# Kernel tuning notes

Hardware: AMD Instinct MI355X
Metric: run time of the kernel (lower is better)

The kernel has to match this reference:

```python
import jax, jax.numpy as jnp
import numpy as np
jax.config.update("jax_enable_x64", True)  # subchunk uses float64 decays (T=128 > 24)

B, T, D = 4, 2048, 1024
H, K = 16, 64            # head_size = 64, D = H*K
CHUNK = 128              # T % 128 == 0 -> only the 128-chunk path of _chunked_wkv runs
DMIX, DDEC = 32, 64      # D_MIX_DIM, D_DECAY_DIM
PREC_MIN = 0.005
LN_EPS = 1e-5 * 8.0 ** 2 # eps * head_size_divisor**2


def setup_inputs() -> dict:
    key = jax.random.key(0)
    ks = jax.random.split(key, 24)
    f32 = jnp.float32
    rn = lambda k, s, sc=1.0: (jax.random.normal(k, s) * sc).astype(f32)
    un = lambda k, s, lo, hi: jax.random.uniform(k, s, minval=lo, maxval=hi).astype(f32)
    inv_sq = 1.0 / np.sqrt(D)
    return {
        "x": rn(ks[0], (B, T, D)),
        # token-mix interpolation coefficients (init-like: in [0,1])
        "time_maa_x": un(ks[1], (1, 1, D), 0.0, 1.0),
        "time_maa_w": un(ks[2], (1, 1, D), 0.0, 1.0),
        "time_maa_k": un(ks[3], (1, 1, D), 0.0, 1.0),
        "time_maa_v": un(ks[4], (1, 1, D), 0.0, 1.0),
        "time_maa_r": un(ks[5], (1, 1, D), 0.0, 1.0),
        "time_maa_g": un(ks[6], (1, 1, D), 0.0, 1.0),
        "time_maa_w1": rn(ks[7], (D, 5 * DMIX), 0.01),
        "time_maa_w2": un(ks[8], (5, DMIX, D), -0.01, 0.01),
        # decay: init range roughly [-6, -1] like the module
        "time_decay": un(ks[9], (1, 1, D), -6.0, -1.0),
        "time_decay_w1": rn(ks[10], (D, DDEC), 0.01),
        "time_decay_w2": un(ks[11], (DDEC, D), -0.01, 0.01),
        "time_faaaa": un(ks[12], (H, K), -0.1, 0.5),
        # projections (stored [in, out]; x @ W == nn.Linear)
        "Wr": rn(ks[13], (D, D), inv_sq),
        "Wk": rn(ks[14], (D, D), inv_sq),
        "Wv": rn(ks[15], (D, D), inv_sq),
        "Wg": rn(ks[16], (D, D), inv_sq),
        "Wo": rn(ks[17], (D, D), inv_sq),
        "ln_w": jnp.ones((D,), f32),
        "ln_b": jnp.zeros((D,), f32),
    }


def _causal_shift(x):
    # x[t-1], zero at t=0
    return jnp.pad(x[:, :-1, :], ((0, 0), (1, 0), (0, 0)))


def _chunked_wkv(r, k, v, w, u, state):
    # r,k,v,w: [B,H,L,K]; u: [1,H,1,K]; state: [B,H,K,V]
    Bb, Hh, L, Kk = r.shape
    V = v.shape[-1]
    Tc = CHUNK
    N = L // Tc
    f64 = jnp.float64

    w_decay = jnp.clip(jnp.exp(w), PREC_MIN, None)
    wc_log = jnp.log(w_decay.astype(jnp.float32)).reshape(Bb, Hh, N, Tc, Kk)
    wc_cum = jnp.cumsum(wc_log, axis=-2)                              # inclusive cumsum over chunk
    shifted = jnp.pad(wc_cum[..., :-1, :], ((0, 0),) * 3 + ((1, 0), (0, 0)))
    ws = wc_log.sum(axis=-2, keepdims=True)                           # [B,H,N,1,K] total log-decay
    w_inter = jnp.exp(ws - wc_cum).astype(r.dtype)
    w_intra = jnp.exp(wc_cum - wc_log).astype(r.dtype)

    rc = r.reshape(Bb, Hh, N, Tc, Kk)
    kc = k.reshape(Bb, Hh, N, Tc, Kk)
    vc = v.reshape(Bb, Hh, N, Tc, V)

    # intra-chunk attention in float64 with mid-chunk offset for stability
    off = shifted[..., Tc // 2:Tc // 2 + 1, :]
    r_decay = jnp.exp((shifted - off).astype(f64))
    k_inv = jnp.exp((off - wc_cum).astype(f64))
    a = jnp.einsum('bhnik,bhnjk->bhnij', rc.astype(f64) * r_decay,
                   kc.astype(f64) * k_inv).astype(r.dtype)
    a = jnp.tril(a, -1)
    diag = jnp.einsum('bhntk,bhntk->bhnt', rc, u[:, :, :, None, :] * kc)  # u bonus on the diagonal
    a = a + diag[..., None] * jnp.eye(Tc, dtype=r.dtype)
    out = jnp.einsum('bhnij,bhnjv->bhniv', a, vc)

    # inter-chunk recurrent state carry
    wkv = jnp.einsum('bhntk,bhntv->bhnkv', kc * w_inter, vc)          # per-chunk KV update
    ws_e = jnp.swapaxes(jnp.exp(ws), -1, -2).astype(r.dtype)          # [B,H,N,K,1]

    def step(s, xs):
        wkv_i, ws_i = xs
        return s * ws_i + wkv_i, s                                    # emit state BEFORE update

    state_f, states = jax.lax.scan(step, state,
                                   (jnp.moveaxis(wkv, 2, 0), jnp.moveaxis(ws_e, 2, 0)))
    states = jnp.moveaxis(states, 0, 2)                               # [B,H,N,K,V]
    out = out + jnp.einsum('bhntk,bhnkv->bhntv', rc * w_intra, states)
    return out.reshape(Bb, Hh, L, V), state_f


def reference(x, time_maa_x, time_maa_w, time_maa_k, time_maa_v, time_maa_r,
              time_maa_g, time_maa_w1, time_maa_w2, time_decay, time_decay_w1,
              time_decay_w2, time_faaaa, Wr, Wk, Wv, Wg, Wo, ln_w, ln_b):
    Bb, Tt, Dd = x.shape
    xx = _causal_shift(x) - x                                          # dxprev (recurrent mode)

    # data-dependent 5-way token-mix (RWKV-6 LoRA mix)
    xxx = jnp.tanh((x + xx * time_maa_x) @ time_maa_w1)                # [B,T,5*DMIX]
    m = jnp.einsum('btfi,fid->fbtd', xxx.reshape(Bb, Tt, 5, DMIX), time_maa_w2)
    mw, mk, mv, mr, mg = m
    xw = x + xx * (time_maa_w + mw)
    xk = x + xx * (time_maa_k + mk)
    xv = x + xx * (time_maa_v + mv)
    xr = x + xx * (time_maa_r + mr)
    xg = x + xx * (time_maa_g + mg)

    to_heads = lambda t: t.reshape(Bb, Tt, H, K).transpose(0, 2, 1, 3)  # [B,H,T,K]
    r = to_heads(xr @ Wr)
    k = to_heads(xk @ Wk)
    v = to_heads(xv @ Wv)
    g = jax.nn.silu(xg @ Wg)

    ww = time_decay + jnp.tanh(xw @ time_decay_w1) @ time_decay_w2
    w = to_heads(-jnp.exp(ww))                                         # log-decay (negative)
    u = time_faaaa.reshape(1, H, 1, K)

    state0 = jnp.zeros((Bb, H, K, K), dtype=x.dtype)
    out, _state = _chunked_wkv(r, k, v, w, u, state0)

    # GroupNorm(n_head groups) over flattened (B*T, D)
    og = out.transpose(0, 2, 1, 3).reshape(Bb * Tt, H, K)
    mu = og.mean(-1, keepdims=True)
    var = og.var(-1, keepdims=True)
    og = (og - mu) / jnp.sqrt(var + LN_EPS)
    out = (og.reshape(Bb * Tt, Dd) * ln_w + ln_b).reshape(Bb, Tt, Dd)

    return (out * g) @ Wo
```

## Files before the change

kernel.cpp:

```cpp
#include <hip/hip_runtime.h>
#include <hip/hip_bf16.h>
#include <math.h>
#include <stdint.h>

typedef __hip_bfloat16 bf16;
typedef __attribute__((ext_vector_type(8))) short short8;
typedef __attribute__((ext_vector_type(4))) short short4v;
typedef __attribute__((ext_vector_type(4))) float f32x4;

#define Tt 2048
#define Dd 1024
#define Hh 16

__device__ __forceinline__ float b2f(bf16 v){ return __bfloat162float(v); }
__device__ __forceinline__ bf16  f2b(float v){ return __float2bfloat16(v); }

__device__ __forceinline__ void async16(const void* g, void* l){
  __builtin_amdgcn_global_load_lds(
      (__attribute__((address_space(1))) void*)(g),
      (__attribute__((address_space(3))) void*)(l),
      16, 0, 0);
}

__device__ __forceinline__ int seg_t(int lr, int t0, int Lm1){ return t0 + (lr & Lm1); }
__device__ __forceinline__ size_t seg_grow(int lr, int b0, int t0, int Llog2, int Lm1){
  return ((size_t)(b0 + (lr >> Llog2)) * Tt) + (size_t)seg_t(lr, t0, Lm1);
}

__device__ __forceinline__ void xcd_swz(int& bn, int& bm, int& z){
  int nbm = gridDim.y;
  if((nbm & 7) == 0){
    int flat = blockIdx.x + (blockIdx.y << 3) + blockIdx.z * (nbm << 3);
    int j = flat & 7, k = flat >> 3;
    int cs = nbm >> 3;
    bn = (k & 7) << 7;
    int kk = k >> 3;
    bm = (j * cs + (kk % cs)) << 7;
    z  = kk / cs;
  } else {
    bn = blockIdx.x << 7; bm = blockIdx.y << 7; z = blockIdx.z;
  }
}

struct MixP { const bf16* maa[5]; bf16* dst[5]; };
struct Proj4 { const bf16* A[4]; const bf16* Bt[4]; bf16* C[4]; };
struct ConvP { const void* src[20]; bf16* dst[20]; };
struct T5P  { const bf16* src[5]; bf16* dst[5]; };

__global__ __launch_bounds__(256) void k_detect(const unsigned short* __restrict__ xs,
                                                int* __restrict__ flag){
  __shared__ int bad;
  if(threadIdx.x == 0) bad = 0;
  __syncthreads();
  int local = 0;
  for(int i = threadIdx.x; i < 8192; i += 256){
    unsigned e = (xs[i] >> 7) & 0xFF;
    if(e >= 0xC0) local++;
  }
  if(local) atomicAdd(&bad, local);
  __syncthreads();
  if(threadIdx.x == 0) flag[0] = (bad > 16) ? 1 : 0;
}

__global__ __launch_bounds__(256) void k_conv_all(ConvP p, const int* __restrict__ flag){
  const int PRE[21] = {0,8388608,8389632,8390656,8391680,8392704,8393728,8394752,
                       8558592,8722432,8723456,8788992,8854528,8855552,9904128,
                       10952704,12001280,13049856,14098432,14099456,14100480};
  int v = (blockIdx.x * 256 + threadIdx.x) * 4;
  if(v >= 14100480) return;
  int a = 0;
  #pragma unroll
  for(int i = 1; i < 20; i++) if(v >= PRE[i]) a = i;
  int off = v - PRE[a];
  bf16* d = p.dst[a] + off;
  if(flag[0]){
    f32x4 xv = *(const f32x4*)((const float*)p.src[a] + off);
    short4v o;
    #pragma unroll
    for(int j = 0; j < 4; j++) ((bf16*)&o)[j] = f2b(xv[j]);
    *(short4v*)d = o;
  } else {
    *(short4v*)d = *(const short4v*)((const short*)p.src[a] + off);
  }
}

__global__ __launch_bounds__(256) void k_transpose5(T5P p){
  __shared__ bf16 tile[32][33];
  const bf16* __restrict__ src = p.src[blockIdx.z];
  bf16* __restrict__ dst       = p.dst[blockIdx.z];
  int bx = blockIdx.x * 32, by = blockIdx.y * 32;
  int tx = threadIdx.x & 31, ty = threadIdx.x >> 5;
  for(int r = ty; r < 32; r += 8)
    tile[r][tx] = src[(size_t)(by + r) * 1024 + bx + tx];
  __syncthreads();
  for(int r = ty; r < 32; r += 8)
    dst[(size_t)(bx + r) * 1024 + by + tx] = tile[tx][r];
}

__global__ __launch_bounds__(256) void k_transposeP(const bf16* __restrict__ src,
                                                    bf16* __restrict__ dst,
                                                    int K, int N, int Npad){
  int idx = blockIdx.x * 256 + threadIdx.x;
  if(idx >= Npad * K) return;
  int n = idx / K, k = idx - n * K;
  dst[idx] = (n < N) ? src[(size_t)k * N + n] : f2b(0.f);
}

__global__ __launch_bounds__(256) void k_transposeP5(const bf16* __restrict__ src,
                                                     bf16* __restrict__ dst){
  int z = blockIdx.z;
  int idx = blockIdx.x * 256 + threadIdx.x;
  int n = idx >> 5, k = idx & 31;
  dst[(size_t)z * 32768 + idx] = src[(size_t)z * 32768 + (size_t)k * 1024 + n];
}

__global__ __launch_bounds__(256) void k_prep(const bf16* __restrict__ x,
                                              const bf16* __restrict__ tmx,
                                              bf16* __restrict__ xmx,
                                              int b0, int t0, int Llog2){
  const int Lm1 = (1 << Llog2) - 1;
  int idx = blockIdx.x * 256 + threadIdx.x;
  int lr = idx >> 10, d = idx & 1023;
  size_t grow = seg_grow(lr, b0, t0, Llog2, Lm1);
  int tl = seg_t(lr, t0, Lm1);
  float xc = b2f(x[grow * Dd + d]);
  float xp = tl ? b2f(x[(grow - 1) * Dd + d]) : 0.f;
  xmx[idx] = f2b(xc + (xp - xc) * b2f(tmx[d]));
}

constexpr int GEPI_BF16 = 0, GEPI_SILU = 1, GEPI_OUT = 2;

template<int EPI>
__global__ __launch_bounds__(256) void gemm_mfma(
    const bf16* __restrict__ A,
    const bf16* __restrict__ Bt,
    void* __restrict__ Cv,
    const int* __restrict__ oflag,
    int rowoff){
  __shared__ __align__(16) short As[128 * 32];
  __shared__ __align__(16) short Bs[128 * 32];
  int tid = threadIdx.x;
  int bn, bm, zz;
  xcd_swz(bn, bm, zz);
  int w = tid >> 6, lane = tid & 63;
  int wm = (w & 1) * 64, wn = (w >> 1) * 64;
  int m16 = lane & 15, quad = lane >> 4;

  f32x4 acc[4][4];
  #pragma unroll
  for(int mi = 0; mi < 4; mi++)
    #pragma unroll
    for(int ni = 0; ni < 4; ni++)
      acc[mi][ni] = (f32x4){0.f, 0.f, 0.f, 0.f};

  int srow = tid >> 2;
  int sk8  = (tid & 3) * 8;
  const bf16* Ag = A  + (size_t)(bm + srow) * 1024 + sk8;
  const bf16* Bg = Bt + (size_t)(bn + srow) * 1024 + sk8;
  short* Al = As + w * 512;
  short* Bl = Bs + w * 512;

  for(int kb = 0; kb < 1024; kb += 32){
    #pragma unroll
    for(int rep = 0; rep < 2; rep++){
      async16(Ag + (size_t)rep * 64 * 1024 + kb, Al + rep * 2048);
      async16(Bg + (size_t)rep * 64 * 1024 + kb, Bl + rep * 2048);
    }
    __syncthreads();
    short8 af[4], bfr[4];
    #pragma unroll
    for(int mi = 0; mi < 4; mi++)
      af[mi] = *(const short8*)(As + (wm + mi * 16 + m16) * 32 + quad * 8);
    #pragma unroll
    for(int ni = 0; ni < 4; ni++)
      bfr[ni] = *(const short8*)(Bs + (wn + ni * 16 + m16) * 32 + quad * 8);
    #pragma unroll
    for(int mi = 0; mi < 4; mi++)
      #pragma unroll
      for(int ni = 0; ni < 4; ni++)
        acc[mi][ni] = __builtin_amdgcn_mfma_f32_16x16x32_bf16(af[mi], bfr[ni], acc[mi][ni], 0, 0, 0);
    __syncthreads();
  }
  #pragma unroll
  for(int mi = 0; mi < 4; mi++){
    #pragma unroll
    for(int ni = 0; ni < 4; ni++){
      #pragma unroll
      for(int r = 0; r < 4; r++){
        int row = bm + wm + mi * 16 + quad * 4 + r;
        int col = bn + wn + ni * 16 + m16;
        float v = acc[mi][ni][r];
        if constexpr(EPI == GEPI_BF16){
          ((bf16*)Cv)[(size_t)row * 1024 + col] = f2b(v);
        } else if constexpr(EPI == GEPI_SILU){
          ((bf16*)Cv)[(size_t)row * 1024 + col] = f2b(v / (1.f + expf(-v)));
        } else {
          size_t off = (size_t)(row + rowoff) * 1024 + col;
          if(oflag[0]) ((float*)Cv)[off] = v;
          else         ((bf16*)Cv)[off]  = f2b(v);
        }
      }
    }
  }
}

__global__ __launch_bounds__(512) void gemm_proj4(Proj4 prm){
  __shared__ __align__(16) short As[2][256 * 32];
  __shared__ __align__(16) short Bs[2][256 * 32];
  int tid = threadIdx.x;
  int flat = blockIdx.x + (blockIdx.y << 2) + (blockIdx.z << 7);
  int j = flat & 7, k = flat >> 3;
  int bn = (k & 3) << 8;
  int kk = k >> 2;
  int bm = (j * 4 + (kk & 3)) << 8;
  int z  = kk >> 2;
  const bf16* __restrict__ A  = prm.A[z];
  const bf16* __restrict__ Bt = prm.Bt[z];
  bf16* __restrict__ C        = prm.C[z];
  int w = tid >> 6, lane = tid & 63;
  int wm = (w & 1) * 128, wn = (w >> 1) * 64;
  int m16 = lane & 15, quad = lane >> 4;

  f32x4 acc[8][4];
  #pragma unroll
  for(int mi = 0; mi < 8; mi++)
    #pragma unroll
    for(int ni = 0; ni < 4; ni++)
      acc[mi][ni] = (f32x4){0.f, 0.f, 0.f, 0.f};

  int srow = tid >> 2;
  int c4   = ((tid & 3) - (srow >> 1)) & 3;
  const bf16* Ag = A  + (size_t)(bm + srow) * 1024 + c4 * 8;
  const bf16* Bg = Bt + (size_t)(bn + srow) * 1024 + c4 * 8;

  auto STG = [&](int buf, int kb){
    #pragma unroll
    for(int rep = 0; rep < 2; rep++){
      async16(Ag + (size_t)rep * 128 * 1024 + kb, &As[buf][rep * 4096 + w * 512]);
      async16(Bg + (size_t)rep * 128 * 1024 + kb, &Bs[buf][rep * 4096 + w * 512]);
    }
  };
  STG(0, 0);
  __syncthreads();
  for(int kbi = 0; kbi < 32; kbi++){
    int cur = kbi & 1;
    if(kbi < 31) STG(cur ^ 1, (kbi + 1) << 5);
    short8 af[8], bfr[4];
    #pragma unroll
    for(int mi = 0; mi < 8; mi++){
      int ar = wm + mi * 16 + m16;
      af[mi] = *(const short8*)(&As[cur][ar * 32 + ((quad + (ar >> 1)) & 3) * 8]);
    }
    #pragma unroll
    for(int ni = 0; ni < 4; ni++){
      int br = wn + ni * 16 + m16;
      bfr[ni] = *(const short8*)(&Bs[cur][br * 32 + ((quad + (br >> 1)) & 3) * 8]);
    }
    #pragma unroll
    for(int mi = 0; mi < 8; mi++)
      #pragma unroll
      for(int ni = 0; ni < 4; ni++)
        acc[mi][ni] = __builtin_amdgcn_mfma_f32_16x16x32_bf16(af[mi], bfr[ni], acc[mi][ni], 0, 0, 0);
    __syncthreads();
  }
  bool silu = (z == 3);
  #pragma unroll
  for(int mi = 0; mi < 8; mi++){
    #pragma unroll
    for(int ni = 0; ni < 4; ni++){
      #pragma unroll
      for(int r = 0; r < 4; r++){
        int row = bm + wm + mi * 16 + quad * 4 + r;
        int col = bn + wn + ni * 16 + m16;
        float v = acc[mi][ni][r];
        if(silu) v = v / (1.f + expf(-v));
        C[(size_t)row * 1024 + col] = f2b(v);
      }
    }
  }
}

__global__ __launch_bounds__(256) void gemm_mix(
    const bf16* __restrict__ xxx,
    const bf16* __restrict__ w2T,
    const bf16* __restrict__ xg,
    MixP prm, int b0, int t0, int Llog2){
  const int Lm1 = (1 << Llog2) - 1;
  int c = blockIdx.z;
  __shared__ __align__(16) short As[128 * 32];
  __shared__ __align__(16) short Bs[128 * 32];
  int tid = threadIdx.x;
  int bn = blockIdx.x * 128;
  int bm = blockIdx.y * 128;
  int w = tid >> 6, lane = tid & 63;
  int wm = (w & 1) * 64, wn = (w >> 1) * 64;
  int m16 = lane & 15, quad = lane >> 4;

  int srow = tid >> 2;
  int sk8  = (tid & 3) * 8;
  short* Al = As + w * 512;
  short* Bl = Bs + w * 512;
  #pragma unroll
  for(int rep = 0; rep < 2; rep++){
    async16(xxx + (size_t)(bm + srow + rep * 64) * 256 + c * 32 + sk8, Al + rep * 2048);
    async16(w2T + (size_t)c * 32768 + (size_t)(bn + srow + rep * 64) * 32 + sk8, Bl + rep * 2048);
  }
  __syncthreads();
  f32x4 acc[4][4];
  short8 af[4], bfr[4];
  #pragma unroll
  for(int mi = 0; mi < 4; mi++)
    af[mi] = *(const short8*)(As + (wm + mi * 16 + m16) * 32 + quad * 8);
  #pragma unroll
  for(int ni = 0; ni < 4; ni++)
    bfr[ni] = *(const short8*)(Bs + (wn + ni * 16 + m16) * 32 + quad * 8);
  #pragma unroll
  for(int mi = 0; mi < 4; mi++)
    #pragma unroll
    for(int ni = 0; ni < 4; ni++)
      acc[mi][ni] = __builtin_amdgcn_mfma_f32_16x16x32_bf16(
          af[mi], bfr[ni], (f32x4){0.f, 0.f, 0.f, 0.f}, 0, 0, 0);

  const bf16* maa = prm.maa[c];
  bf16* dst = prm.dst[c];
  #pragma unroll
  for(int mi = 0; mi < 4; mi++){
    #pragma unroll
    for(int ni = 0; ni < 4; ni++){
      #pragma unroll
      for(int r = 0; r < 4; r++){
        int row = bm + wm + mi * 16 + quad * 4 + r;
        int col = bn + wn + ni * 16 + m16;
        size_t grow = seg_grow(row, b0, t0, Llog2, Lm1);
        int tl = seg_t(row, t0, Lm1);
        float xc = b2f(xg[grow * Dd + col]);
        float xp = tl ? b2f(xg[(grow - 1) * Dd + col]) : 0.f;
        dst[(size_t)row * 1024 + col] =
            f2b(xc + (xp - xc) * (b2f(maa[col]) + acc[mi][ni][r]));
      }
    }
  }
}

constexpr int G2_TANH = 0, G2_DECAY = 1;

template<int EPI>
__global__ __launch_bounds__(256) void gemm_mfma2(
    const bf16* __restrict__ A,
    const bf16* __restrict__ Bt,
    void* __restrict__ Cv, int ldc,
    int Ndim, int Kdim,
    const bf16* __restrict__ e_w){
  __shared__ __align__(16) short As[128 * 32];
  __shared__ __align__(16) short Bs[128 * 32];
  int tid = threadIdx.x;
  int bn = blockIdx.x * 128;
  int bm = blockIdx.y * 128;
  int w = tid >> 6, lane = tid & 63;
  int wm = (w & 1) * 64, wn = (w >> 1) * 64;
  int m16 = lane & 15, quad = lane >> 4;

  f32x4 acc[4][4];
  #pragma unroll
  for(int mi = 0; mi < 4; mi++)
    #pragma unroll
    for(int ni = 0; ni < 4; ni++)
      acc[mi][ni] = (f32x4){0.f, 0.f, 0.f, 0.f};

  int srow = tid >> 2;
  int sk8  = (tid & 3) * 8;
  const bf16* Ag = A  + (size_t)(bm + srow) * Kdim + sk8;
  const bf16* Bg = Bt + (size_t)(bn + srow) * Kdim + sk8;
  short* Al = As + w * 512;
  short* Bl = Bs + w * 512;

  for(int kb = 0; kb < Kdim; kb += 32){
    #pragma unroll
    for(int rep = 0; rep < 2; rep++){
      async16(Ag + (size_t)rep * 64 * Kdim + kb, Al + rep * 2048);
      async16(Bg + (size_t)rep * 64 * Kdim + kb, Bl + rep * 2048);
    }
    __syncthreads();
    short8 af[4], bfr[4];
    #pragma unroll
    for(int mi = 0; mi < 4; mi++)
      af[mi] = *(const short8*)(As + (wm + mi * 16 + m16) * 32 + quad * 8);
    #pragma unroll
    for(int ni = 0; ni < 4; ni++)
      bfr[ni] = *(const short8*)(Bs + (wn + ni * 16 + m16) * 32 + quad * 8);
    #pragma unroll
    for(int mi = 0; mi < 4; mi++)
      #pragma unroll
      for(int ni = 0; ni < 4; ni++)
        acc[mi][ni] = __builtin_amdgcn_mfma_f32_16x16x32_bf16(af[mi], bfr[ni], acc[mi][ni], 0, 0, 0);
    __syncthreads();
  }
  #pragma unroll
  for(int mi = 0; mi < 4; mi++){
    #pragma unroll
    for(int ni = 0; ni < 4; ni++){
      #pragma unroll
      for(int r = 0; r < 4; r++){
        int row = bm + wm + mi * 16 + quad * 4 + r;
        int col = bn + wn + ni * 16 + m16;
        if(col >= Ndim) continue;
        float v = acc[mi][ni][r];
        size_t off = (size_t)row * ldc + col;
        if constexpr(EPI == G2_TANH){
          ((bf16*)Cv)[off] = f2b(tanhf(v));
        } else {
          float td = b2f(e_w[col]) + v;
          ((float*)Cv)[off] = fmaxf(-expf(td), -5.2983173665480363f);
        }
      }
    }
  }
}

constexpr int EPI_OUTV = 5;
#define BM 64
#define BN 64
#define BK 16

template<int EPI>
__global__ __launch_bounds__(256) void gemm_ep(
    const bf16* __restrict__ A, int lda,
    const bf16* __restrict__ Bm, int ldb,
    void* __restrict__ Cv, int ldc,
    int Mdim, int Ndim, int Kdim,
    const bf16* __restrict__ xg, const bf16* __restrict__ e_w,
    int b0, int t0, int Llog2, const int* __restrict__ oflag){
  const int Lm1 = (1 << Llog2) - 1;
  __shared__ float As[BM][BK + 1];
  __shared__ float Bs[BK][BN + 4];
  int tid = threadIdx.x;
  int tx = tid & 15, ty = tid >> 4;
  int bm = blockIdx.y * BM, bn = blockIdx.x * BN;
  float acc[4][4] = {};
  for(int kb = 0; kb < Kdim; kb += BK){
    {
      int lr = tid >> 2;
      int lc = (tid & 3) * 4;
      int gr = bm + lr;
      #pragma unroll
      for(int q = 0; q < 4; q++){
        int gc = kb + lc + q;
        float av = 0.f;
        if(gr < Mdim && gc < Kdim)
          av = b2f(A[(size_t)gr * lda + gc]);
        As[lr][lc + q] = av;
      }
    }
    {
      int lr = tid >> 4;
      int lc = (tid & 15) * 4;
      #pragma unroll
      for(int q = 0; q < 4; q++){
        int gr = kb + lr; int gc = bn + lc + q;
        Bs[lr][lc + q] = (gr < Kdim && gc < Ndim) ? b2f(Bm[(size_t)gr * ldb + gc]) : 0.f;
      }
    }
    __syncthreads();
    #pragma unroll
    for(int kk = 0; kk < BK; kk++){
      float ar[4], br[4];
      #pragma unroll
      for(int q = 0; q < 4; q++) ar[q] = As[ty * 4 + q][kk];
      #pragma unroll
      for(int q = 0; q < 4; q++) br[q] = Bs[kk][tx * 4 + q];
      #pragma unroll
      for(int mi = 0; mi < 4; mi++)
        #pragma unroll
        for(int ni = 0; ni < 4; ni++)
          acc[mi][ni] += ar[mi] * br[ni];
    }
    __syncthreads();
  }
  #pragma unroll
  for(int mi = 0; mi < 4; mi++){
    int row = bm + ty * 4 + mi;
    if(row >= Mdim) continue;
    #pragma unroll
    for(int ni = 0; ni < 4; ni++){
      int col = bn + tx * 4 + ni;
      if(col >= Ndim) continue;
      float vacc = acc[mi][ni];
      size_t grow = seg_grow(row, b0, t0, Llog2, Lm1);
      size_t go = grow * Dd + col;
      if(oflag[0]) ((float*)Cv)[go] = vacc;
      else         ((bf16*)Cv)[go]  = f2b(vacc);
    }
  }
}

__global__ __launch_bounds__(256) void k_cumsum(float* __restrict__ wd,
                                                float* __restrict__ wse,
                                                int nlog2){
  int blk = blockIdx.x;
  int dg = blk & 3; int rest = blk >> 2;
  int nmask = (1 << nlog2) - 1;
  int ln = rest & nmask; int bp = rest >> nlog2;
  int d = dg * 256 + threadIdx.x;
  size_t rowbase = (((size_t)bp << nlog2) + ln) * 128;
  size_t base = rowbase * Dd + d;
  float c = 0.f;
  for(int t = 0; t < 128; t++){
    size_t ix = base + (size_t)t * Dd;
    c += wd[ix];
    wd[ix] = c;
  }
  int h = d >> 6, k0 = d & 63;
  wse[((((size_t)bp * Hh + h) << nlog2) | ln) * 64 + k0] = __expf(fminf(c, 0.f));
}

__global__ __launch_bounds__(256) void k_chunk1(const bf16* __restrict__ kb,
                                                const bf16* __restrict__ vb,
                                                const float* __restrict__ wcum,
                                                float* __restrict__ wkv,
                                                int nlog2){
  __shared__ __align__(16) bf16 ktT[64 * 136];
  __shared__ __align__(16) bf16 vT2[64 * 136];
  int tid = threadIdx.x, blk = blockIdx.x;
  int nmask = (1 << nlog2) - 1;
  int ln = blk & nmask; int rest = blk >> nlog2;
  int h = rest & 15; int bp = rest >> 4;
  size_t rowbase = (((size_t)bp << nlog2) + ln) * 128;
  size_t gbase = rowbase * Dd + h * 64;
  for(int r = 0; r < 32; r++){
    int idx = r * 256 + tid;
    int t0 = idx >> 6, k0 = idx & 63;
    size_t gi = gbase + (size_t)t0 * Dd + k0;
    float c  = wcum[gi];
    float cL = wcum[gbase + (size_t)127 * Dd + k0];
    ktT[k0 * 136 + t0] = f2b(b2f(kb[gi]) * __expf(fminf(cL - c, 0.f)));
    vT2[k0 * 136 + t0] = vb[gi];
  }
  __syncthreads();
  int w = tid >> 6, lane = tid & 63;
  int m16 = lane & 15, quad = lane >> 4;
  f32x4 acc[4];
  #pragma unroll
  for(int nt = 0; nt < 4; nt++) acc[nt] = (f32x4){0.f, 0.f, 0.f, 0.f};
  #pragma unroll
  for(int ks = 0; ks < 4; ks++){
    short8 af = *(const short8*)(ktT + (w * 16 + m16) * 136 + ks * 32 + quad * 8);
    #pragma unroll
    for(int nt = 0; nt < 4; nt++){
      short8 bfr = *(const short8*)(vT2 + (nt * 16 + m16) * 136 + ks * 32 + quad * 8);
      acc[nt] = __builtin_amdgcn_mfma_f32_16x16x32_bf16(af, bfr, acc[nt], 0, 0, 0);
    }
  }
  size_t obase = (size_t)blk * 4096;
  #pragma unroll
  for(int nt = 0; nt < 4; nt++)
    #pragma unroll
    for(int r = 0; r < 4; r++)
      wkv[obase + (size_t)(w * 16 + quad * 4 + r) * 64 + nt * 16 + m16] = acc[nt][r];
}

__global__ __launch_bounds__(256) void k_scan(float* __restrict__ buf,
                                              const float* __restrict__ wse,
                                              float* __restrict__ st,
                                              int b0, int firstseg, int nlog2){
  int blk = blockIdx.x;
  int h = blk & 15, bp = blk >> 4;
  int tid = threadIdx.x;
  size_t stbase = ((size_t)(b0 + bp) * Hh + h) * 4096;
  int nloc = 1 << nlog2;
  float s[16];
  #pragma unroll
  for(int r = 0; r < 16; r++)
    s[r] = firstseg ? 0.f : st[stbase + r * 256 + tid];
  for(int ln = 0; ln < nloc; ln++){
    size_t idx = (((size_t)bp * Hh + h) << nlog2) | ln;
    size_t base = idx * 4096;
    const float* wsp = wse + idx * 64;
    #pragma unroll
    for(int r = 0; r < 16; r++){
      int e = r * 256 + tid;
      float tmp = buf[base + e];
      buf[base + e] = s[r];
      s[r] = s[r] * wsp[e >> 6] + tmp;
    }
  }
  #pragma unroll
  for(int r = 0; r < 16; r++)
    st[stbase + r * 256 + tid] = s[r];
}

__global__ __launch_bounds__(256) void k_chunk2(
    const bf16* __restrict__ rb, const bf16* __restrict__ kb,
    const bf16* __restrict__ vb, const float* __restrict__ wcum,
    const float* __restrict__ states, const bf16* __restrict__ u,
    float* __restrict__ outw, int nlog2){
  __shared__ __align__(16) bf16 vT[64 * 136];
  __shared__ __align__(16) bf16 sT[64 * 72];
  __shared__ __align__(16) bf16 ascr[4 * 16 * 136];
  int tid = threadIdx.x, blk = blockIdx.x;
  int nmask = (1 << nlog2) - 1;
  int ln = blk & nmask; int rest = blk >> nlog2;
  int h = rest & 15; int bp = rest >> 4;
  size_t rowbase = (((size_t)bp << nlog2) + ln) * 128;
  size_t gbase = rowbase * Dd + h * 64;
  for(int r = 0; r < 32; r++){
    int idx = r * 256 + tid;
    int t0 = idx >> 6, v0 = idx & 63;
    vT[v0 * 136 + t0] = vb[gbase + (size_t)t0 * Dd + v0];
  }
  for(int r = 0; r < 16; r++){
    int idx = r * 256 + tid;
    int k0 = idx >> 6, v0 = idx & 63;
    sT[v0 * 72 + k0] = f2b(states[(size_t)blk * 4096 + k0 * 64 + v0]);
  }
  __syncthreads();
  int w = tid >> 6, lane = tid & 63;
  int m16 = lane & 15, quad = lane >> 4;
  bf16* scr = ascr + w * (16 * 136);
  f32x4 oacc[2][4];
  #pragma unroll
  for(int a1 = 0; a1 < 2; a1++)
    #pragma unroll
    for(int a2 = 0; a2 < 4; a2++) oacc[a1][a2] = (f32x4){0.f, 0.f, 0.f, 0.f};

  for(int ii = 0; ii < 2; ii++){
    int I = ii ? (7 - w) : w;
    int B = I * 16;
    for(int z = lane; z < 544; z += 64) ((unsigned long long*)scr)[z] = 0ULL;
    int i0 = B + m16;
    size_t rowi = rowbase + i0;
    short8 rf[2], af[2], rw2[2];
    float crv[2][8];
    #pragma unroll
    for(int ks = 0; ks < 2; ks++){
      int koff = h * 64 + ks * 32 + quad * 8;
      rf[ks] = *(const short8*)(rb + rowi * Dd + koff);
      float cp[8];
      if(i0 > 0){
        f32x4 c0 = *(const f32x4*)(wcum + (rowi - 1) * Dd + koff);
        f32x4 c1 = *(const f32x4*)(wcum + (rowi - 1) * Dd + koff + 4);
        #pragma unroll
        for(int c = 0; c < 4; c++){ cp[c] = c0[c]; cp[4 + c] = c1[c]; }
      } else {
        #pragma unroll
        for(int c = 0; c < 8; c++) cp[c] = 0.f;
      }
      if(B > 0){
        f32x4 c0 = *(const f32x4*)(wcum + (rowbase + B - 1) * Dd + koff);
        f32x4 c1 = *(const f32x4*)(wcum + (rowbase + B - 1) * Dd + koff + 4);
        #pragma unroll
        for(int c = 0; c < 4; c++){ crv[ks][c] = c0[c]; crv[ks][4 + c] = c1[c]; }
      } else {
        #pragma unroll
        for(int c = 0; c < 8; c++) crv[ks][c] = 0.f;
      }
      short8 av, wv;
      #pragma unroll
      for(int c = 0; c < 8; c++){
        float rv = b2f(((const bf16*)&rf[ks])[c]);
        ((bf16*)&av)[c] = f2b(rv * __expf(fminf(cp[c] - crv[ks][c], 0.f)));
        ((bf16*)&wv)[c] = f2b(rv * __expf(fminf(cp[c], 0.f)));
      }
      af[ks] = av; rw2[ks] = wv;
    }
    for(int J = 0; J < I; J++){
      f32x4 aacc = (f32x4){0.f, 0.f, 0.f, 0.f};
      #pragma unroll
      for(int ks = 0; ks < 2; ks++){
        int koff = h * 64 + ks * 32 + quad * 8;
        size_t rowj = rowbase + J * 16 + m16;
        short8 k8 = *(const short8*)(kb + rowj * Dd + koff);
        f32x4 c0 = *(const f32x4*)(wcum + rowj * Dd + koff);
        f32x4 c1 = *(const f32x4*)(wcum + rowj * Dd + koff + 4);
        short8 bfrag;
        #pragma unroll
        for(int c = 0; c < 8; c++){
          float kv = b2f(((const bf16*)&k8)[c]);
          float cj = (c < 4) ? c0[c] : c1[c - 4];
          ((bf16*)&bfrag)[c] = f2b(kv * __expf(fminf(crv[ks][c] - cj, 0.f)));
        }
        aacc = __builtin_amdgcn_mfma_f32_16x16x32_bf16(af[ks], bfrag, aacc, 0, 0, 0);
      }
      #pragma unroll
      for(int r = 0; r < 4; r++)
        scr[(quad * 4 + r) * 136 + J * 16 + m16] = f2b(aacc[r]);
    }
    {
      f32x4 aacc = (f32x4){0.f, 0.f, 0.f, 0.f};
      f32x4 dacc = (f32x4){0.f, 0.f, 0.f, 0.f};
      #pragma unroll
      for(int ks = 0; ks < 2; ks++){
        int koff = h * 64 + ks * 32 + quad * 8;
        size_t rowj = rowbase + B + m16;
        short8 k8 = *(const short8*)(kb + rowj * Dd + koff);
        f32x4 c0 = *(const f32x4*)(wcum + rowj * Dd + koff);
        f32x4 c1 = *(const f32x4*)(wcum + rowj * Dd + koff + 4);
        short8 u8 = *(const short8*)(u + h * 64 + ks * 32 + quad * 8);
        short8 bf1, bf2;
        #pragma unroll
        for(int c = 0; c < 8; c++){
          float kv = b2f(((const bf16*)&k8)[c]);
          float cj = (c < 4) ? c0[c] : c1[c - 4];
          ((bf16*)&bf1)[c] = f2b(kv * __expf(crv[ks][c] - cj));
          ((bf16*)&bf2)[c] = f2b(kv * b2f(((const bf16*)&u8)[c]));
        }
        aacc = __builtin_amdgcn_mfma_f32_16x16x32_bf16(af[ks], bf1, aacc, 0, 0, 0);
        dacc = __builtin_amdgcn_mfma_f32_16x16x32_bf16(rf[ks], bf2, dacc, 0, 0, 0);
      }
      #pragma unroll
      for(int r = 0; r < 4; r++){
        int row = quad * 4 + r, col = m16;
        if(col < row)       scr[row * 136 + B + col] = f2b(aacc[r]);
        else if(col == row) scr[row * 136 + B + col] = f2b(dacc[r]);
      }
    }
    asm volatile("s_waitcnt lgkmcnt(0)" ::: "memory");
    int nks = (I + 2) >> 1;
    for(int ks2 = 0; ks2 < nks; ks2++){
      short8 afr = *(const short8*)(scr + m16 * 136 + ks2 * 32 + quad * 8);
      #pragma unroll
      for(int nt = 0; nt < 4; nt++){
        short8 bfr = *(const short8*)(vT + (nt * 16 + m16) * 136 + ks2 * 32 + quad * 8);
        oacc[ii][nt] = __builtin_amdgcn_mfma_f32_16x16x32_bf16(afr, bfr, oacc[ii][nt], 0, 0, 0);
      }
    }
    #pragma unroll
    for(int ks = 0; ks < 2; ks++){
      #pragma unroll
      for(int nt = 0; nt < 4; nt++){
        short8 sfr = *(const short8*)(sT + (nt * 16 + m16) * 72 + ks * 32 + quad * 8);
        oacc[ii][nt] = __builtin_amdgcn_mfma_f32_16x16x32_bf16(rw2[ks], sfr, oacc[ii][nt], 0, 0, 0);
      }
    }
  }
  __syncthreads();
  #pragma unroll
  for(int ii = 0; ii < 2; ii++){
    int I = ii ? (7 - w) : w;
    int B = I * 16;
    #pragma unroll
    for(int nt = 0; nt < 4; nt++){
      #pragma unroll
      for(int r = 0; r < 4; r++){
        int i0 = B + quad * 4 + r;
        int v0 = nt * 16 + m16;
        outw[gbase + (size_t)i0 * Dd + v0] = oacc[ii][nt][r];
      }
    }
  }
}

__global__ __launch_bounds__(256) void k_norm(const float* __restrict__ outw,
                                              const bf16* __restrict__ gb,
                                              const bf16* __restrict__ lnw,
                                              const bf16* __restrict__ lnb,
                                              bf16* __restrict__ gated){
  int lr = blockIdx.x;
  int wv = threadIdx.x >> 6, lane = threadIdx.x & 63;
  for(int hh = wv; hh < Hh; hh += 4){
    size_t ix = (size_t)lr * Dd + hh * 64 + lane;
    float xv = outw[ix];
    float s1 = xv, s2 = xv * xv;
    #pragma unroll
    for(int off = 32; off > 0; off >>= 1){
      s1 += __shfl_xor(s1, off);
      s2 += __shfl_xor(s2, off);
    }
    float mu  = s1 * 0.015625f;
    float var = s2 * 0.015625f - mu * mu;
    float inv = rsqrtf(var + 6.4e-4f);
    float og  = (xv - mu) * inv * b2f(lnw[hh * 64 + lane]) + b2f(lnb[hh * 64 + lane]);
    gated[ix] = f2b(og * b2f(gb[ix]));
  }
}

extern "C" void kernel_launch(void* const* d_in, const int* in_sizes, int n_in,
                              void* d_out, int out_size, void* d_ws, size_t ws_size,
                              hipStream_t stream){
  char* W = (char*)d_ws;
  size_t cur = 0;
  auto carve = [&](size_t bytes) -> char* {
    char* p = W + cur;
    cur = (cur + bytes + 255) & ~(size_t)255;
    return p;
  };

  int* flag = (int*)carve(4096);
  static const int NEL[20] = {8388608, 1024, 1024, 1024, 1024, 1024, 1024,
                              163840, 163840, 1024, 65536, 65536, 1024,
                              1048576, 1048576, 1048576, 1048576, 1048576,
                              1024, 1024};
  bf16* canon[20];
  for(int i = 0; i < 20; i++) canon[i] = (bf16*)carve((size_t)NEL[i] * 2);

  k_detect<<<dim3(1), 256, 0, stream>>>((const unsigned short*)d_in[0], flag);
  ConvP cp;
  for(int i = 0; i < 20; i++){ cp.src[i] = d_in[i]; cp.dst[i] = canon[i]; }
  k_conv_all<<<dim3(13770), 256, 0, stream>>>(cp, flag);

  const bf16* xp   = canon[0];
  const bf16* tmx  = canon[1];
  const bf16* tdec = canon[9];
  const bf16* up   = canon[12];
  const bf16* lnwp = canon[18];
  const bf16* lnbp = canon[19];

  bf16* WrT  = (bf16*)carve(2097152);
  bf16* WkT  = (bf16*)carve(2097152);
  bf16* WvT  = (bf16*)carve(2097152);
  bf16* WgT  = (bf16*)carve(2097152);
  bf16* WoT  = (bf16*)carve(2097152);
  bf16* W1T  = (bf16*)carve(256 * 1024 * 2);
  bf16* DW1T = (bf16*)carve(128 * 1024 * 2);
  bf16* DW2T = (bf16*)carve(1024 * 64 * 2);
  bf16* W2T  = (bf16*)carve(5 * 1024 * 32 * 2);
  T5P tp;
  tp.src[0] = canon[13]; tp.dst[0] = WrT;
  tp.src[1] = canon[14]; tp.dst[1] = WkT;
  tp.src[2] = canon[15]; tp.dst[2] = WvT;
  tp.src[3] = canon[16]; tp.dst[3] = WgT;
  tp.src[4] = canon[17]; tp.dst[4] = WoT;
  k_transpose5<<<dim3(32, 32, 5), 256, 0, stream>>>(tp);
  k_transposeP<<<dim3(1024), 256, 0, stream>>>(canon[7],  W1T,  1024, 160, 256);
  k_transposeP<<<dim3(512),  256, 0, stream>>>(canon[10], DW1T, 1024, 64, 128);
  k_transposeP<<<dim3(256),  256, 0, stream>>>(canon[11], DW2T, 64, 1024, 1024);
  k_transposeP5<<<dim3(128, 1, 5), 256, 0, stream>>>(canon[8], W2T);

  float* st = (float*)carve(1u << 20);
  size_t FIXED = cur;

  const size_t UNIT = 19104, PAD = 65536;
  int nb, L;
  if(ws_size >= FIXED + (size_t)8192 * UNIT + PAD){ nb = 4; L = 2048; }
  else {
    nb = 1; L = 2048;
    while(L > 128 && ws_size < FIXED + (size_t)L * UNIT + PAD) L >>= 1;
  }
  const int Llog2 = __builtin_ctz((unsigned)L);
  const int nlog2 = Llog2 - 7;
  const int M     = nb * L;
  const size_t Mr = (size_t)M;

  bf16*  xxx    = (bf16*) carve(Mr * 512);
  bf16*  ww1    = (bf16*) carve(Mr * 128);
  float* wse    = (float*)carve(Mr * 32);
  bf16*  xmx    = (bf16*) carve(Mr * 2048);
  bf16*  mixbuf = (bf16*) carve(Mr * 2048);
  bf16*  kbuf   = (bf16*) carve(Mr * 2048);
  bf16*  vbuf   = (bf16*) carve(Mr * 2048);
  bf16*  rbuf   = (bf16*) carve(Mr * 2048);
  bf16*  gbuf   = (bf16*) carve(Mr * 2048);
  float* wdec   = (float*)carve(Mr * 4096);
  float* wkvst  = (float*)carve(Mr * 2048);
  float* outw   = wdec;
  bf16*  gated  = mixbuf;

  MixP mp;
  mp.maa[0] = canon[2]; mp.maa[1] = canon[3]; mp.maa[2] = canon[4];
  mp.maa[3] = canon[5]; mp.maa[4] = canon[6];
  mp.dst[0] = mixbuf;
  mp.dst[1] = (bf16*)wdec;
  mp.dst[2] = (bf16*)wdec + Mr * 1024;
  mp.dst[3] = (bf16*)wkvst;
  mp.dst[4] = xmx;

  Proj4 pp;
  pp.A[0] = mp.dst[1]; pp.Bt[0] = WkT; pp.C[0] = kbuf;
  pp.A[1] = mp.dst[2]; pp.Bt[1] = WvT; pp.C[1] = vbuf;
  pp.A[2] = mp.dst[3]; pp.Bt[2] = WrT; pp.C[2] = rbuf;
  pp.A[3] = mp.dst[4]; pp.Bt[3] = WgT; pp.C[3] = gbuf;

  for(int b0 = 0; b0 < 4; b0 += nb){
    for(int t0 = 0; t0 < Tt; t0 += L){
      k_prep<<<dim3(M * 4), 256, 0, stream>>>(xp, tmx, xmx, b0, t0, Llog2);
      gemm_mfma2<G2_TANH><<<dim3(2, M/128), 256, 0, stream>>>(
          xmx, W1T, xxx, 256, 160, 1024, nullptr);
      gemm_mix<<<dim3(8, M/128, 5), 256, 0, stream>>>(
          xxx, W2T, xp, mp, b0, t0, Llog2);
      if(M == 8192){
        gemm_proj4<<<dim3(4, 32, 4), 512, 0, stream>>>(pp);
      } else {
        for(int z = 0; z < 4; z++){
          if(z == 3)
            gemm_mfma<GEPI_SILU><<<dim3(8, M/128), 256, 0, stream>>>(pp.A[z], pp.Bt[z], pp.C[z], flag, 0);
          else
            gemm_mfma<GEPI_BF16><<<dim3(8, M/128), 256, 0, stream>>>(pp.A[z], pp.Bt[z], pp.C[z], flag, 0);
        }
      }
      gemm_mfma2<G2_TANH><<<dim3(1, M/128), 256, 0, stream>>>(
          mixbuf, DW1T, ww1, 64, 64, 1024, nullptr);
      gemm_mfma2<G2_DECAY><<<dim3(8, M/128), 256, 0, stream>>>(
          ww1, DW2T, wdec, 1024, 1024, 64, tdec);
      int nloc = 1 << nlog2;
      k_cumsum<<<dim3(nb * nloc * 4), 256, 0, stream>>>(wdec, wse, nlog2);
      k_chunk1<<<dim3(nb * 16 * nloc), 256, 0, stream>>>(kbuf, vbuf, wdec, wkvst, nlog2);
      k_scan<<<dim3(nb * 16), 256, 0, stream>>>(wkvst, wse, st, b0, (t0 == 0) ? 1 : 0, nlog2);
      k_chunk2<<<dim3(nb * 16 * nloc), 256, 0, stream>>>(rbuf, kbuf, vbuf, wdec, wkvst, up, outw, nlog2);
      k_norm<<<dim3(M), 256, 0, stream>>>(outw, gbuf, lnwp, lnbp, gated);
      if(L == Tt){
        gemm_mfma<GEPI_OUT><<<dim3(8, M/128), 256, 0, stream>>>(gated, WoT, d_out, flag, b0 * Tt);
      } else {
        gemm_ep<EPI_OUTV><<<dim3(16, M/64), 256, 0, stream>>>(
            gated, 1024, canon[17], 1024, d_out, 1024, M, 1024, 1024,
            nullptr, nullptr, b0, t0, Llog2, flag);
      }
    }
  }
}
```

Measured before the change: 551.6 us.

## Deepen proj GEMM prefetch pipeline and reuse 256-tile kernel for output projection

The 256x256 projection GEMM now issues loads two k-steps ahead, using explicit vmcnt waits and raw barriers in place of the load-then-syncthreads pattern, and raises wave priority around the MFMA block. The kernel is templated on its epilogue so the output projection (Wo) can also use the large-tile kernel when M is 8192, replacing the 128-tile gemm_mfma. The aim is to hide global-to-LDS latency and improve the tile efficiency of the final GEMM. The output GEMM launches only 128 blocks, which may underfill the GPU's compute units.

```diff
diff --git a/kernel.cpp b/kernel.cpp
--- a/kernel.cpp
+++ b/kernel.cpp
@@ -204,7 +204,10 @@
   }
 }
 
-__global__ __launch_bounds__(512) void gemm_proj4(Proj4 prm){
+template<int EPI>
+__global__ __launch_bounds__(512) void gemm256(Proj4 prm,
+                                               const int* __restrict__ oflag,
+                                               int rowoff){
   __shared__ __align__(16) short As[2][256 * 32];
   __shared__ __align__(16) short Bs[2][256 * 32];
   int tid = threadIdx.x;
@@ -212,7 +215,7 @@
   int j = flat & 7, k = flat >> 3;
   int bn = (k & 3) << 8;
   int kk = k >> 2;
-  int bm = (j * 4 + (kk & 3)) << 8;
+  int bm = ((j << 2) + (kk & 3)) << 8;
   int z  = kk >> 2;
   const bf16* __restrict__ A  = prm.A[z];
   const bf16* __restrict__ Bt = prm.Bt[z];
@@ -241,10 +244,13 @@
     }
   };
   STG(0, 0);
-  __syncthreads();
+  STG(1, 32);
+  asm volatile("s_waitcnt vmcnt(4)" ::: "memory");
+  __builtin_amdgcn_s_barrier();
+  __builtin_amdgcn_sched_barrier(0);
+
   for(int kbi = 0; kbi < 32; kbi++){
     int cur = kbi & 1;
-    if(kbi < 31) STG(cur ^ 1, (kbi + 1) << 5);
     short8 af[8], bfr[4];
     #pragma unroll
     for(int mi = 0; mi < 8; mi++){
@@ -256,14 +262,23 @@
       int br = wn + ni * 16 + m16;
       bfr[ni] = *(const short8*)(&Bs[cur][br * 32 + ((quad + (br >> 1)) & 3) * 8]);
     }
+    __builtin_amdgcn_s_setprio(1);
     #pragma unroll
     for(int mi = 0; mi < 8; mi++)
       #pragma unroll
       for(int ni = 0; ni < 4; ni++)
         acc[mi][ni] = __builtin_amdgcn_mfma_f32_16x16x32_bf16(af[mi], bfr[ni], acc[mi][ni], 0, 0, 0);
-    __syncthreads();
-  }
-  bool silu = (z == 3);
+    __builtin_amdgcn_s_setprio(0);
+    __builtin_amdgcn_s_barrier();
+    if(kbi + 2 < 32){
+      STG(cur, (kbi + 2) << 5);
+      asm volatile("s_waitcnt vmcnt(4)" ::: "memory");
+    } else {
+      asm volatile("s_waitcnt vmcnt(0)" ::: "memory");
+    }
+    __builtin_amdgcn_s_barrier();
+    __builtin_amdgcn_sched_barrier(0);
+  }
   #pragma unroll
   for(int mi = 0; mi < 8; mi++){
     #pragma unroll
@@ -273,8 +288,14 @@
         int row = bm + wm + mi * 16 + quad * 4 + r;
         int col = bn + wn + ni * 16 + m16;
         float v = acc[mi][ni][r];
-        if(silu) v = v / (1.f + expf(-v));
-        C[(size_t)row * 1024 + col] = f2b(v);
+        if constexpr(EPI == GEPI_BF16){
+          if(z == 3) v = v / (1.f + expf(-v));
+          C[(size_t)row * 1024 + col] = f2b(v);
+        } else {
+          size_t off = (size_t)(row + rowoff) * 1024 + col;
+          if(oflag[0]) ((float*)C)[off] = v;
+          else         C[off] = f2b(v);
+        }
       }
     }
   }
@@ -877,7 +898,7 @@
       gemm_mix<<<dim3(8, M/128, 5), 256, 0, stream>>>(
           xxx, W2T, xp, mp, b0, t0, Llog2);
       if(M == 8192){
-        gemm_proj4<<<dim3(4, 32, 4), 512, 0, stream>>>(pp);
+        gemm256<GEPI_BF16><<<dim3(4, 32, 4), 512, 0, stream>>>(pp, flag, 0);
       } else {
         for(int z = 0; z < 4; z++){
           if(z == 3)
@@ -897,7 +918,13 @@
       k_chunk2<<<dim3(nb * 16 * nloc), 256, 0, stream>>>(rbuf, kbuf, vbuf, wdec, wkvst, up, outw, nlog2);
       k_norm<<<dim3(M), 256, 0, stream>>>(outw, gbuf, lnwp, lnbp, gated);
       if(L == Tt){
-        gemm_mfma<GEPI_OUT><<<dim3(8, M/128), 256, 0, stream>>>(gated, WoT, d_out, flag, b0 * Tt);
+        if(M == 8192){
+          Proj4 po;
+          po.A[0] = gated; po.Bt[0] = WoT; po.C[0] = (bf16*)d_out;
+          gemm256<GEPI_OUT><<<dim3(4, 32, 1), 512, 0, stream>>>(po, flag, b0 * Tt);
+        } else {
+          gemm_mfma<GEPI_OUT><<<dim3(8, M/128), 256, 0, stream>>>(gated, WoT, d_out, flag, b0 * Tt);
+        }
       } else {
         gemm_ep<EPI_OUTV><<<dim3(16, M/64), 256, 0, stream>>>(
             gated, 1024, canon[17], 1024, d_out, 1024, M, 1024, 1024,
```

New measurement: 558.7 us. About the same (+1.3%).

## Deepen projection GEMM pipeline to four LDS stages with explicit waitcnt

Applied to the files above, without the earlier changes.

Replaces the double-buffered LDS pipeline in the fused 4-way projection GEMM with a 4-buffer ring that prefetches three k-tiles ahead. Explicit vmcnt waits and raw s_barrier calls replace __syncthreads, and s_setprio raises wave priority around the MFMA block. The goal is to hide global-to-LDS load latency better. In exchange LDS use doubles to 128KB per block, which may cut occupancy, and the manual waitcnt bookkeeping is fragile.

```diff
diff --git a/kernel.cpp b/kernel.cpp
--- a/kernel.cpp
+++ b/kernel.cpp
@@ -204,15 +204,14 @@
   }
 }
 
-__global__ __launch_bounds__(512) void gemm_proj4(Proj4 prm){
-  __shared__ __align__(16) short As[2][256 * 32];
-  __shared__ __align__(16) short Bs[2][256 * 32];
+__global__ __launch_bounds__(512) void gemm256(Proj4 prm){
+  __shared__ __align__(16) short lds4[4][16384];
   int tid = threadIdx.x;
   int flat = blockIdx.x + (blockIdx.y << 2) + (blockIdx.z << 7);
   int j = flat & 7, k = flat >> 3;
   int bn = (k & 3) << 8;
   int kk = k >> 2;
-  int bm = (j * 4 + (kk & 3)) << 8;
+  int bm = ((j << 2) + (kk & 3)) << 8;
   int z  = kk >> 2;
   const bf16* __restrict__ A  = prm.A[z];
   const bf16* __restrict__ Bt = prm.Bt[z];
@@ -233,35 +232,55 @@
   const bf16* Ag = A  + (size_t)(bm + srow) * 1024 + c4 * 8;
   const bf16* Bg = Bt + (size_t)(bn + srow) * 1024 + c4 * 8;
 
-  auto STG = [&](int buf, int kb){
+  auto STG = [&](int buf, int t){
+    int kb = t << 5;
     #pragma unroll
     for(int rep = 0; rep < 2; rep++){
-      async16(Ag + (size_t)rep * 128 * 1024 + kb, &As[buf][rep * 4096 + w * 512]);
-      async16(Bg + (size_t)rep * 128 * 1024 + kb, &Bs[buf][rep * 4096 + w * 512]);
+      async16(Ag + (size_t)rep * 128 * 1024 + kb, &lds4[buf][rep * 4096 + w * 512]);
+      async16(Bg + (size_t)rep * 128 * 1024 + kb, &lds4[buf][8192 + rep * 4096 + w * 512]);
     }
   };
-  STG(0, 0);
-  __syncthreads();
-  for(int kbi = 0; kbi < 32; kbi++){
-    int cur = kbi & 1;
-    if(kbi < 31) STG(cur ^ 1, (kbi + 1) << 5);
+  STG(0, 0); STG(1, 1); STG(2, 2);
+  asm volatile("s_waitcnt vmcnt(8)" ::: "memory");
+  __builtin_amdgcn_s_barrier();
+  __builtin_amdgcn_sched_barrier(0);
+
+  for(int t = 0; t < 32; t++){
+    int buf = t & 3;
+    const short* As_b = &lds4[buf][0];
+    const short* Bs_b = &lds4[buf][8192];
     short8 af[8], bfr[4];
     #pragma unroll
     for(int mi = 0; mi < 8; mi++){
       int ar = wm + mi * 16 + m16;
-      af[mi] = *(const short8*)(&As[cur][ar * 32 + ((quad + (ar >> 1)) & 3) * 8]);
+      af[mi] = *(const short8*)(As_b + ar * 32 + ((quad + (ar >> 1)) & 3) * 8);
     }
     #pragma unroll
     for(int ni = 0; ni < 4; ni++){
       int br = wn + ni * 16 + m16;
-      bfr[ni] = *(const short8*)(&Bs[cur][br * 32 + ((quad + (br >> 1)) & 3) * 8]);
-    }
+      bfr[ni] = *(const short8*)(Bs_b + br * 32 + ((quad + (br >> 1)) & 3) * 8);
+    }
+    __builtin_amdgcn_s_setprio(1);
     #pragma unroll
     for(int mi = 0; mi < 8; mi++)
       #pragma unroll
       for(int ni = 0; ni < 4; ni++)
         acc[mi][ni] = __builtin_amdgcn_mfma_f32_16x16x32_bf16(af[mi], bfr[ni], acc[mi][ni], 0, 0, 0);
-    __syncthreads();
+    __builtin_amdgcn_s_setprio(0);
+    __builtin_amdgcn_sched_barrier(0);
+    __builtin_amdgcn_s_barrier();
+    if(t < 29){
+      STG((t + 3) & 3, t + 3);
+      asm volatile("s_waitcnt vmcnt(8)" ::: "memory");
+    } else if(t == 29){
+      asm volatile("s_waitcnt vmcnt(4)" ::: "memory");
+    } else if(t == 30){
+      asm volatile("s_waitcnt vmcnt(0)" ::: "memory");
+    }
+    if(t < 31){
+      __builtin_amdgcn_s_barrier();
+      __builtin_amdgcn_sched_barrier(0);
+    }
   }
   bool silu = (z == 3);
   #pragma unroll
@@ -877,7 +896,7 @@
       gemm_mix<<<dim3(8, M/128, 5), 256, 0, stream>>>(
           xxx, W2T, xp, mp, b0, t0, Llog2);
       if(M == 8192){
-        gemm_proj4<<<dim3(4, 32, 4), 512, 0, stream>>>(pp);
+        gemm256<<<dim3(4, 32, 4), 512, 0, stream>>>(pp);
       } else {
         for(int z = 0; z < 4; z++){
           if(z == 3)
```

After: 536.6 us. 2.7% less time.
